# Optimization experiments

Hardware: AMD Instinct MI355X
Metric: run time of the kernel (lower is better)

The kernel has to match this reference:

```python
import jax, jax.numpy as jnp
import numpy as np

N_NODES = 50000
N_EDGES = 600000
DIM = 128
BN_EPS = 1e-5


def _gine_conv(x, src, dst, edge_attr, W, b):
    # message: relu(x_j + e_ij), gathered from source nodes
    m = jax.nn.relu(x[src] + edge_attr)              # [E, D]
    aggr = jax.ops.segment_sum(m, dst, num_segments=x.shape[0])  # [N, D]
    # eps = 0 (PyG default, train_eps=False): (1+eps)*x + aggr
    return (x + aggr) @ W.T + b


def _batchnorm(x, gamma, beta):
    mean = jnp.mean(x, axis=0)
    var = jnp.var(x, axis=0)
    return (x - mean) * jax.lax.rsqrt(var + BN_EPS) * gamma + beta


def setup_inputs() -> dict:
    key = jax.random.key(0)
    ks = jax.random.split(key, 16)
    scale = 1.0 / np.sqrt(DIM)
    inp = {
        "edge_index": jax.random.randint(ks[0], (2, N_EDGES), 0, N_NODES, dtype=jnp.int64 if jax.config.jax_enable_x64 else jnp.int32),
        "node_attr": jax.random.normal(ks[1], (N_NODES, DIM), dtype=jnp.float32),
        "edge_attr": jax.random.normal(ks[2], (N_EDGES, DIM), dtype=jnp.float32),
    }
    for i in range(3):
        inp[f"W{i+1}"] = jax.random.uniform(ks[3 + i], (DIM, DIM), jnp.float32, -scale, scale)
        inp[f"b{i+1}"] = jax.random.uniform(ks[6 + i], (DIM,), jnp.float32, -scale, scale)
        inp[f"gamma{i+1}"] = jnp.ones((DIM,), jnp.float32)
        inp[f"beta{i+1}"] = jnp.zeros((DIM,), jnp.float32)
    return inp


def reference(edge_index, node_attr, edge_attr,
              W1, b1, gamma1, beta1,
              W2, b2, gamma2, beta2,
              W3, b3, gamma3, beta3):
    src, dst = edge_index[0], edge_index[1]
    x = jax.nn.relu(_gine_conv(node_attr, src, dst, edge_attr, W1, b1))
    x = _batchnorm(x, gamma1, beta1)
    x = jax.nn.relu(_gine_conv(x, src, dst, edge_attr, W2, b2))
    x = _batchnorm(x, gamma2, beta2)
    x = jax.nn.relu(_gine_conv(x, src, dst, edge_attr, W3, b3))
    x = _batchnorm(x, gamma3, beta3)
    return x
```

## Files before the change

### kernel.cpp

```cpp
#include <hip/hip_runtime.h>
#include <stdint.h>

#define NN 50000
#define NE 600000
#define DIM 128
#define BN_EPS 1e-5f
#define NCHUNK ((NN + 255) / 256)

typedef __attribute__((ext_vector_type(8))) short bf16x8;
typedef __attribute__((ext_vector_type(4))) float f32x4;

__device__ __forceinline__ unsigned short f2b(float f) {
    unsigned u = __float_as_uint(f);
    u += 0x7FFF + ((u >> 16) & 1);
    return (unsigned short)(u >> 16);
}
__device__ __forceinline__ float b2f(unsigned short h) {
    return __uint_as_float((unsigned)h << 16);
}


__global__ __launch_bounds__(256) void zero_k(int* __restrict__ counts,
                                              double* __restrict__ gsum,
                                              double* __restrict__ gsumsq) {
    int i = blockIdx.x * 256 + threadIdx.x;
    if (i < NN) counts[i] = 0;
    if (i < DIM) { gsum[i] = 0.0; gsumsq[i] = 0.0; }
}

__global__ void count_k(const int* __restrict__ dst, int* __restrict__ counts, int E) {
    int i = blockIdx.x * 256 + threadIdx.x;
    if (i < E) atomicAdd(&counts[dst[i]], 1);
}

__global__ __launch_bounds__(256) void chunksum_k(const int* __restrict__ counts,
                                                  int* __restrict__ bsum) {
    __shared__ int lds[256];
    int i = blockIdx.x * 256 + threadIdx.x;
    lds[threadIdx.x] = (i < NN) ? counts[i] : 0;
    __syncthreads();
    for (int off = 128; off > 0; off >>= 1) {
        if (threadIdx.x < (unsigned)off) lds[threadIdx.x] += lds[threadIdx.x + off];
        __syncthreads();
    }
    if (threadIdx.x == 0) bsum[blockIdx.x] = lds[0];
}

__global__ __launch_bounds__(256) void chunkscan_k(const int* __restrict__ bsum,
                                                   int* __restrict__ bbase,
                                                   int* __restrict__ offsets) {
    __shared__ int lds[256];
    int t = threadIdx.x;
    int v = (t < NCHUNK) ? bsum[t] : 0;
    lds[t] = v;
    __syncthreads();
    for (int off = 1; off < 256; off <<= 1) {
        int a = (t >= (unsigned)off) ? lds[t - off] : 0;
        __syncthreads();
        lds[t] += a;
        __syncthreads();
    }
    if (t < NCHUNK) bbase[t] = lds[t] - v;
    if (t == 0) offsets[NN] = NE;
}

__global__ __launch_bounds__(256) void scatteroff_k(const int* __restrict__ counts,
                                                    const int* __restrict__ bbase,
                                                    int* __restrict__ offsets,
                                                    int* __restrict__ cursor) {
    __shared__ int lds[256];
    int t = threadIdx.x;
    int i = blockIdx.x * 256 + t;
    int v = (i < NN) ? counts[i] : 0;
    lds[t] = v;
    __syncthreads();
    for (int off = 1; off < 256; off <<= 1) {
        int a = (t >= (unsigned)off) ? lds[t - off] : 0;
        __syncthreads();
        lds[t] += a;
        __syncthreads();
    }
    if (i < NN) {
        int excl = bbase[blockIdx.x] + lds[t] - v;
        offsets[i] = excl;
        cursor[i] = excl;
    }
}

template <bool WEBF>
__global__ __launch_bounds__(256) void fillcvt_k(
        const int* __restrict__ dst, const int* __restrict__ src,
        const float* __restrict__ eattr, int* __restrict__ cursor,
        int* __restrict__ csrc, int* __restrict__ eidx,
        unsigned short* __restrict__ ebf) {
    int lane = threadIdx.x & 31;
    int g = blockIdx.x * 8 + (threadIdx.x >> 5);
    int base = g * 32;
    if (base >= NE) return;
    int i = base + lane;
    int d = dst[i];
    int p = atomicAdd(&cursor[d], 1);
    csrc[p] = src[i];
    if (!WEBF) { eidx[p] = i; return; }
    int f = lane * 4;
    for (int t = 0; t < 32; ++t) {
        int pt = __shfl(p, t, 32);
        float4 v = *(const float4*)(eattr + (size_t)(base + t) * DIM + f);
        ushort4 o = {f2b(v.x), f2b(v.y), f2b(v.z), f2b(v.w)};
        *(ushort4*)(ebf + (size_t)pt * DIM + f) = o;
    }
}

__global__ __launch_bounds__(256) void wcvt_k(const float* __restrict__ w0,
                                              const float* __restrict__ w1,
                                              const float* __restrict__ w2,
                                              unsigned short* __restrict__ whi,
                                              unsigned short* __restrict__ wlo) {
    int i = blockIdx.x * 256 + threadIdx.x;
    int which = i >> 12;
    int off = (i & 4095) * 4;
    const float* w = (which == 0) ? w0 : ((which == 1) ? w1 : w2);
    float4 v = *(const float4*)(w + off);
    ushort4 h = {f2b(v.x), f2b(v.y), f2b(v.z), f2b(v.w)};
    ushort4 l = {f2b(v.x - b2f(h.x)), f2b(v.y - b2f(h.y)),
                 f2b(v.z - b2f(h.z)), f2b(v.w - b2f(h.w))};
    *(ushort4*)(whi + (size_t)which * 16384 + off) = h;
    *(ushort4*)(wlo + (size_t)which * 16384 + off) = l;
}

template <int XMODE, int EMODE>
__global__ __launch_bounds__(256) void layer_k(
        const float* __restrict__ xf, const unsigned short* __restrict__ xb,
        const float* __restrict__ scale, const float* __restrict__ shift,
        const unsigned short* __restrict__ ebf, const float* __restrict__ eattr,
        const int* __restrict__ eidx, const int* __restrict__ offsets,
        const int* __restrict__ csrc,
        const unsigned short* __restrict__ whi, const unsigned short* __restrict__ wlo,
        const float* __restrict__ bias, unsigned short* __restrict__ yb,
        double* __restrict__ gsum, double* __restrict__ gsumsq) {
    __shared__ float sS[16][DIM + 4];
    __shared__ unsigned short ylds[16][136];

    int tid = threadIdx.x;
    int lane31 = tid & 31;
    int grp = tid >> 5;
    int n0 = blockIdx.x * 16;
    int f = lane31 * 4;

    float4 sc, sh;
    if (XMODE) {
        sc = *(const float4*)(scale + f);
        sh = *(const float4*)(shift + f);
    }

#pragma unroll
    for (int sub = 0; sub < 2; ++sub) {
        int n = n0 + grp * 2 + sub;
        float4 acc = make_float4(0.f, 0.f, 0.f, 0.f);
        int beg = offsets[n], end = offsets[n + 1];
        for (int b = beg; b < end; b += 32) {
            int kk = b + lane31;
            int s_l = (kk < end) ? csrc[kk] : 0;
            int e_l = 0;
            if (EMODE == 1) e_l = (kk < end) ? eidx[kk] : 0;
            int cnt = end - b;
            if (cnt > 32) cnt = 32;
#pragma unroll 4
            for (int t = 0; t < cnt; ++t) {
                int s = __shfl(s_l, t, 32);
                float4 ev;
                if (EMODE == 0) {
                    ushort4 eb = *(const ushort4*)(ebf + (size_t)(b + t) * DIM + f);
                    ev = make_float4(b2f(eb.x), b2f(eb.y), b2f(eb.z), b2f(eb.w));
                } else {
                    int e = __shfl(e_l, t, 32);
                    ev = *(const float4*)(eattr + (size_t)e * DIM + f);
                }
                float4 xv;
                if (XMODE == 0) {
                    xv = *(const float4*)(xf + (size_t)s * DIM + f);
                } else {
                    ushort4 u = *(const ushort4*)(xb + (size_t)s * DIM + f);
                    xv = make_float4(fmaf(b2f(u.x), sc.x, sh.x),
                                     fmaf(b2f(u.y), sc.y, sh.y),
                                     fmaf(b2f(u.z), sc.z, sh.z),
                                     fmaf(b2f(u.w), sc.w, sh.w));
                }
                acc.x += fmaxf(xv.x + ev.x, 0.f);
                acc.y += fmaxf(xv.y + ev.y, 0.f);
                acc.z += fmaxf(xv.z + ev.z, 0.f);
                acc.w += fmaxf(xv.w + ev.w, 0.f);
            }
        }
        float4 xn;
        if (XMODE == 0) {
            xn = *(const float4*)(xf + (size_t)n * DIM + f);
        } else {
            ushort4 u = *(const ushort4*)(xb + (size_t)n * DIM + f);
            xn = make_float4(fmaf(b2f(u.x), sc.x, sh.x), fmaf(b2f(u.y), sc.y, sh.y),
                             fmaf(b2f(u.z), sc.z, sh.z), fmaf(b2f(u.w), sc.w, sh.w));
        }
        float4 o = make_float4(xn.x + acc.x, xn.y + acc.y, xn.z + acc.z, xn.w + acc.w);
        *(float4*)(&sS[grp * 2 + sub][f]) = o;
    }
    __syncthreads();

    int wv = tid >> 6;
    int lane = tid & 63;
    int row = lane & 15;
    int kg = lane >> 4;
    int d0 = wv * 32;
    const unsigned short* bh = whi + (size_t)(d0 + row) * DIM + kg * 8;
    const unsigned short* bl = wlo + (size_t)(d0 + row) * DIM + kg * 8;

    f32x4 acc0 = {0.f, 0.f, 0.f, 0.f};
    f32x4 acc1 = {0.f, 0.f, 0.f, 0.f};
#pragma unroll
    for (int ks = 0; ks < 4; ++ks) {
        const float* ap = &sS[row][kg * 8 + ks * 32];
        bf16x8 a;
#pragma unroll
        for (int j = 0; j < 8; ++j) a[j] = (short)f2b(ap[j]);
        bf16x8 b0h = *(const bf16x8*)(bh + ks * 32);
        bf16x8 b0l = *(const bf16x8*)(bl + ks * 32);
        bf16x8 b1h = *(const bf16x8*)(bh + 16 * DIM + ks * 32);
        bf16x8 b1l = *(const bf16x8*)(bl + 16 * DIM + ks * 32);
        acc0 = __builtin_amdgcn_mfma_f32_16x16x32_bf16(a, b0h, acc0, 0, 0, 0);
        acc0 = __builtin_amdgcn_mfma_f32_16x16x32_bf16(a, b0l, acc0, 0, 0, 0);
        acc1 = __builtin_amdgcn_mfma_f32_16x16x32_bf16(a, b1h, acc1, 0, 0, 0);
        acc1 = __builtin_amdgcn_mfma_f32_16x16x32_bf16(a, b1l, acc1, 0, 0, 0);
    }

    float bias0 = bias[d0 + row];
    float bias1 = bias[d0 + 16 + row];
    float s0 = 0.f, q0 = 0.f, s1 = 0.f, q1 = 0.f;
#pragma unroll
    for (int r = 0; r < 4; ++r) {
        int m = kg * 4 + r;
        float y0 = fmaxf(acc0[r] + bias0, 0.f);
        float y1 = fmaxf(acc1[r] + bias1, 0.f);
        ylds[m][d0 + row] = f2b(y0);
        ylds[m][d0 + 16 + row] = f2b(y1);
        s0 += y0; q0 += y0 * y0;
        s1 += y1; q1 += y1 * y1;
    }
    s0 += __shfl_xor(s0, 16); s0 += __shfl_xor(s0, 32);
    q0 += __shfl_xor(q0, 16); q0 += __shfl_xor(q0, 32);
    s1 += __shfl_xor(s1, 16); s1 += __shfl_xor(s1, 32);
    q1 += __shfl_xor(q1, 16); q1 += __shfl_xor(q1, 32);
    if (kg == 0) {
        atomicAdd(&gsum[d0 + row], (double)s0);
        atomicAdd(&gsumsq[d0 + row], (double)q0);
        atomicAdd(&gsum[d0 + 16 + row], (double)s1);
        atomicAdd(&gsumsq[d0 + 16 + row], (double)q1);
    }
    __syncthreads();
    int nrow = tid >> 4, seg = tid & 15;
    *(float4*)(yb + (size_t)(n0 + nrow) * DIM + seg * 8) =
        *(const float4*)(&ylds[nrow][seg * 8]);
}

__global__ void finalize_k(double* __restrict__ gsum, double* __restrict__ gsumsq,
                           const float* __restrict__ gamma, const float* __restrict__ beta,
                           float* __restrict__ scale, float* __restrict__ shift) {
    int d = threadIdx.x;
    if (d < DIM) {
        double mean = gsum[d] * (1.0 / NN);
        double var = gsumsq[d] * (1.0 / NN) - mean * mean;
        float sc = gamma[d] * rsqrtf((float)var + BN_EPS);
        scale[d] = sc;
        shift[d] = beta[d] - (float)mean * sc;
        gsum[d] = 0.0;
        gsumsq[d] = 0.0;
    }
}

__global__ __launch_bounds__(256) void norm_out_k(
        const unsigned short* __restrict__ yb, const float* __restrict__ scale,
        const float* __restrict__ shift, float* __restrict__ out) {
    int i = blockIdx.x * 256 + threadIdx.x;
    int f = (i & 31) * 4;
    ushort4 y = *(const ushort4*)(yb + (size_t)i * 4);
    float4 sc = *(const float4*)(scale + f);
    float4 sh = *(const float4*)(shift + f);
    float4 o;
    o.x = fmaf(b2f(y.x), sc.x, sh.x);
    o.y = fmaf(b2f(y.y), sc.y, sh.y);
    o.z = fmaf(b2f(y.z), sc.z, sh.z);
    o.w = fmaf(b2f(y.w), sc.w, sh.w);
    ((float4*)out)[i] = o;
}


extern "C" void kernel_launch(void* const* d_in, const int* in_sizes, int n_in,
                              void* d_out, int out_size, void* d_ws, size_t ws_size,
                              hipStream_t stream) {
    const int* edge_index = (const int*)d_in[0];
    const int* srcs = edge_index;
    const int* dsts = edge_index + NE;
    const float* node_attr = (const float*)d_in[1];
    const float* eattr = (const float*)d_in[2];
    const float* Wp[3]    = {(const float*)d_in[3],  (const float*)d_in[7],  (const float*)d_in[11]};
    const float* bp[3]    = {(const float*)d_in[4],  (const float*)d_in[8],  (const float*)d_in[12]};
    const float* gammap[3]= {(const float*)d_in[5],  (const float*)d_in[9],  (const float*)d_in[13]};
    const float* betap[3] = {(const float*)d_in[6],  (const float*)d_in[10], (const float*)d_in[14]};

    size_t off = 0;
    char* base = (char*)d_ws;
    auto carve = [&](size_t bytes) -> void* {
        void* p = base + off;
        off += (bytes + 255) & ~(size_t)255;
        return p;
    };
    unsigned short* ybufA = (unsigned short*)carve((size_t)NN * DIM * 2);
    unsigned short* ybufB = (unsigned short*)carve((size_t)NN * DIM * 2);
    int* csrc    = (int*)carve((size_t)NE * 4);
    int* eidx    = (int*)carve((size_t)NE * 4);
    int* offsets = (int*)carve((size_t)(NN + 1) * 4);
    int* cursor  = (int*)carve((size_t)NN * 4);
    int* bsum    = (int*)carve((size_t)NCHUNK * 4);
    int* bbase   = (int*)carve((size_t)NCHUNK * 4);
    int* counts  = (int*)carve((size_t)NN * 4);
    double* gsum = (double*)carve(DIM * 8);
    double* gsumsq = (double*)carve(DIM * 8);
    float* scb   = (float*)carve(3 * DIM * 4);
    float* shb   = (float*)carve(3 * DIM * 4);
    unsigned short* whi = (unsigned short*)carve(3 * DIM * DIM * 2);
    unsigned short* wlo = (unsigned short*)carve(3 * DIM * DIM * 2);
    int use_ebf = (off + (size_t)NE * DIM * 2 <= ws_size);
    unsigned short* ebf = use_ebf ? (unsigned short*)carve((size_t)NE * DIM * 2) : nullptr;

    zero_k<<<NCHUNK, 256, 0, stream>>>(counts, gsum, gsumsq);
    count_k<<<(NE + 255) / 256, 256, 0, stream>>>(dsts, counts, NE);
    chunksum_k<<<NCHUNK, 256, 0, stream>>>(counts, bsum);
    chunkscan_k<<<1, 256, 0, stream>>>(bsum, bbase, offsets);
    scatteroff_k<<<NCHUNK, 256, 0, stream>>>(counts, bbase, offsets, cursor);
    if (use_ebf)
        fillcvt_k<true><<<(NE / 32 + 7) / 8, 256, 0, stream>>>(dsts, srcs, eattr, cursor,
                                                               csrc, eidx, ebf);
    else
        fillcvt_k<false><<<(NE / 32 + 7) / 8, 256, 0, stream>>>(dsts, srcs, eattr, cursor,
                                                                csrc, eidx, nullptr);
    wcvt_k<<<48, 256, 0, stream>>>(Wp[0], Wp[1], Wp[2], whi, wlo);

    if (use_ebf)
        layer_k<0, 0><<<NN / 16, 256, 0, stream>>>(node_attr, nullptr, nullptr, nullptr,
                                                   ebf, eattr, eidx, offsets, csrc,
                                                   whi, wlo, bp[0], ybufA, gsum, gsumsq);
    else
        layer_k<0, 1><<<NN / 16, 256, 0, stream>>>(node_attr, nullptr, nullptr, nullptr,
                                                   nullptr, eattr, eidx, offsets, csrc,
                                                   whi, wlo, bp[0], ybufA, gsum, gsumsq);
    finalize_k<<<1, DIM, 0, stream>>>(gsum, gsumsq, gammap[0], betap[0], scb, shb);

    unsigned short* xin = ybufA;
    unsigned short* yout = ybufB;
    for (int l = 1; l < 3; ++l) {
        const float* sc = scb + (l - 1) * DIM;
        const float* sh = shb + (l - 1) * DIM;
        if (use_ebf)
            layer_k<1, 0><<<NN / 16, 256, 0, stream>>>(nullptr, xin, sc, sh,
                                                       ebf, eattr, eidx, offsets, csrc,
                                                       whi + l * DIM * DIM, wlo + l * DIM * DIM,
                                                       bp[l], yout, gsum, gsumsq);
        else
            layer_k<1, 1><<<NN / 16, 256, 0, stream>>>(nullptr, xin, sc, sh,
                                                       nullptr, eattr, eidx, offsets, csrc,
                                                       whi + l * DIM * DIM, wlo + l * DIM * DIM,
                                                       bp[l], yout, gsum, gsumsq);
        finalize_k<<<1, DIM, 0, stream>>>(gsum, gsumsq, gammap[l], betap[l],
                                          scb + l * DIM, shb + l * DIM);
        unsigned short* t = xin; xin = yout; yout = t;
    }
    norm_out_k<<<NN * DIM / 4 / 256, 256, 0, stream>>>(xin, scb + 2 * DIM, shb + 2 * DIM,
                                                       (float*)d_out);
}
```

Measured before the change: 491.8 us.

## Fuse BN finalize into layer kernels, merge init kernels, prequantize node features

Drops the per-layer finalize kernels. Each layer kernel, and the output kernel, now recompute the batch-norm scale and shift from per-layer double sums, which are kept in separate buffers so nothing has to be zeroed again. The zero and weight-convert kernels merge into one init kernel, which also converts node_attr to bf16 so the first layer gathers half the bytes. Edge loads and stores use nontemporal hints. The cost is redundant stats computation in every thread, and bf16 rounding of the first layer's input, which changes precision.

```diff
diff --git a/kernel.cpp b/kernel.cpp
--- a/kernel.cpp
+++ b/kernel.cpp
@@ -6,9 +6,11 @@
 #define DIM 128
 #define BN_EPS 1e-5f
 #define NCHUNK ((NN + 255) / 256)
+#define NABBLK (NN * DIM / 4 / 256)
 
 typedef __attribute__((ext_vector_type(8))) short bf16x8;
 typedef __attribute__((ext_vector_type(4))) float f32x4;
+typedef __attribute__((ext_vector_type(2))) unsigned int u32x2;
 
 __device__ __forceinline__ unsigned short f2b(float f) {
     unsigned u = __float_as_uint(f);
@@ -20,13 +22,42 @@
 }
 
 
-__global__ __launch_bounds__(256) void zero_k(int* __restrict__ counts,
+__global__ __launch_bounds__(256) void init_k(int* __restrict__ counts,
                                               double* __restrict__ gsum,
-                                              double* __restrict__ gsumsq) {
-    int i = blockIdx.x * 256 + threadIdx.x;
-    if (i < NN) counts[i] = 0;
-    if (i < DIM) { gsum[i] = 0.0; gsumsq[i] = 0.0; }
-}
+                                              double* __restrict__ gsumsq,
+                                              const float* __restrict__ w0,
+                                              const float* __restrict__ w1,
+                                              const float* __restrict__ w2,
+                                              unsigned short* __restrict__ whi,
+                                              unsigned short* __restrict__ wlo,
+                                              const float* __restrict__ xf,
+                                              unsigned short* __restrict__ nabf) {
+    int bid = blockIdx.x;
+    if (bid < NCHUNK) {
+        int i = bid * 256 + threadIdx.x;
+        if (i < NN) counts[i] = 0;
+        if (i < 3 * DIM) { gsum[i] = 0.0; gsumsq[i] = 0.0; }
+    } else if (bid < NCHUNK + 48) {
+        int i = (bid - NCHUNK) * 256 + threadIdx.x;
+        int which = i >> 12;
+        int off = (i & 4095) * 4;
+        const float* w = (which == 0) ? w0 : ((which == 1) ? w1 : w2);
+        float4 v = *(const float4*)(w + off);
+        ushort4 h = {f2b(v.x), f2b(v.y), f2b(v.z), f2b(v.w)};
+        ushort4 l = {f2b(v.x - b2f(h.x)), f2b(v.y - b2f(h.y)),
+                     f2b(v.z - b2f(h.z)), f2b(v.w - b2f(h.w))};
+        *(ushort4*)(whi + (size_t)which * 16384 + off) = h;
+        *(ushort4*)(wlo + (size_t)which * 16384 + off) = l;
+    } else {
+        int idx = (bid - NCHUNK - 48) * 256 + threadIdx.x;
+        f32x4 v = __builtin_nontemporal_load((const f32x4*)(xf + (size_t)idx * 4));
+        u32x2 o;
+        o[0] = (unsigned)f2b(v[0]) | ((unsigned)f2b(v[1]) << 16);
+        o[1] = (unsigned)f2b(v[2]) | ((unsigned)f2b(v[3]) << 16);
+        __builtin_nontemporal_store(o, (u32x2*)(nabf + (size_t)idx * 4));
+    }
+}
+
 
 __global__ void count_k(const int* __restrict__ dst, int* __restrict__ counts, int E) {
     int i = blockIdx.x * 256 + threadIdx.x;
@@ -103,41 +134,29 @@
     csrc[p] = src[i];
     if (!WEBF) { eidx[p] = i; return; }
     int f = lane * 4;
+#pragma unroll 4
     for (int t = 0; t < 32; ++t) {
         int pt = __shfl(p, t, 32);
-        float4 v = *(const float4*)(eattr + (size_t)(base + t) * DIM + f);
-        ushort4 o = {f2b(v.x), f2b(v.y), f2b(v.z), f2b(v.w)};
-        *(ushort4*)(ebf + (size_t)pt * DIM + f) = o;
-    }
-}
-
-__global__ __launch_bounds__(256) void wcvt_k(const float* __restrict__ w0,
-                                              const float* __restrict__ w1,
-                                              const float* __restrict__ w2,
-                                              unsigned short* __restrict__ whi,
-                                              unsigned short* __restrict__ wlo) {
-    int i = blockIdx.x * 256 + threadIdx.x;
-    int which = i >> 12;
-    int off = (i & 4095) * 4;
-    const float* w = (which == 0) ? w0 : ((which == 1) ? w1 : w2);
-    float4 v = *(const float4*)(w + off);
-    ushort4 h = {f2b(v.x), f2b(v.y), f2b(v.z), f2b(v.w)};
-    ushort4 l = {f2b(v.x - b2f(h.x)), f2b(v.y - b2f(h.y)),
-                 f2b(v.z - b2f(h.z)), f2b(v.w - b2f(h.w))};
-    *(ushort4*)(whi + (size_t)which * 16384 + off) = h;
-    *(ushort4*)(wlo + (size_t)which * 16384 + off) = l;
+        f32x4 v = __builtin_nontemporal_load(
+            (const f32x4*)(eattr + (size_t)(base + t) * DIM + f));
+        u32x2 o;
+        o[0] = (unsigned)f2b(v[0]) | ((unsigned)f2b(v[1]) << 16);
+        o[1] = (unsigned)f2b(v[2]) | ((unsigned)f2b(v[3]) << 16);
+        __builtin_nontemporal_store(o, (u32x2*)(ebf + (size_t)pt * DIM + f));
+    }
 }
 
 template <int XMODE, int EMODE>
 __global__ __launch_bounds__(256) void layer_k(
-        const float* __restrict__ xf, const unsigned short* __restrict__ xb,
-        const float* __restrict__ scale, const float* __restrict__ shift,
+        const unsigned short* __restrict__ xb,
+        const double* __restrict__ gs_prev, const double* __restrict__ gq_prev,
+        const float* __restrict__ gamma_prev, const float* __restrict__ beta_prev,
         const unsigned short* __restrict__ ebf, const float* __restrict__ eattr,
         const int* __restrict__ eidx, const int* __restrict__ offsets,
         const int* __restrict__ csrc,
         const unsigned short* __restrict__ whi, const unsigned short* __restrict__ wlo,
         const float* __restrict__ bias, unsigned short* __restrict__ yb,
-        double* __restrict__ gsum, double* __restrict__ gsumsq) {
+        double* __restrict__ gs_cur, double* __restrict__ gq_cur) {
     __shared__ float sS[16][DIM + 4];
     __shared__ unsigned short ylds[16][136];
 
@@ -147,10 +166,17 @@
     int n0 = blockIdx.x * 16;
     int f = lane31 * 4;
 
-    float4 sc, sh;
-    if (XMODE) {
-        sc = *(const float4*)(scale + f);
-        sh = *(const float4*)(shift + f);
+    f32x4 sc, sh;
+    if (XMODE == 1) {
+#pragma unroll
+        for (int j = 0; j < 4; ++j) {
+            int d = f + j;
+            double mean = gs_prev[d] * (1.0 / NN);
+            double var = gq_prev[d] * (1.0 / NN) - mean * mean;
+            float s = gamma_prev[d] * rsqrtf((float)var + BN_EPS);
+            sc[j] = s;
+            sh[j] = beta_prev[d] - (float)mean * s;
+        }
     }
 
 #pragma unroll
@@ -170,21 +196,25 @@
                 int s = __shfl(s_l, t, 32);
                 float4 ev;
                 if (EMODE == 0) {
-                    ushort4 eb = *(const ushort4*)(ebf + (size_t)(b + t) * DIM + f);
-                    ev = make_float4(b2f(eb.x), b2f(eb.y), b2f(eb.z), b2f(eb.w));
+                    u32x2 ew = __builtin_nontemporal_load(
+                        (const u32x2*)(ebf + (size_t)(b + t) * DIM + f));
+                    ev = make_float4(b2f((unsigned short)(ew[0] & 0xFFFFu)),
+                                     b2f((unsigned short)(ew[0] >> 16)),
+                                     b2f((unsigned short)(ew[1] & 0xFFFFu)),
+                                     b2f((unsigned short)(ew[1] >> 16)));
                 } else {
                     int e = __shfl(e_l, t, 32);
                     ev = *(const float4*)(eattr + (size_t)e * DIM + f);
                 }
+                ushort4 u = *(const ushort4*)(xb + (size_t)s * DIM + f);
                 float4 xv;
-                if (XMODE == 0) {
-                    xv = *(const float4*)(xf + (size_t)s * DIM + f);
+                if (XMODE == 1) {
+                    xv = make_float4(fmaf(b2f(u.x), sc[0], sh[0]),
+                                     fmaf(b2f(u.y), sc[1], sh[1]),
+                                     fmaf(b2f(u.z), sc[2], sh[2]),
+                                     fmaf(b2f(u.w), sc[3], sh[3]));
                 } else {
-                    ushort4 u = *(const ushort4*)(xb + (size_t)s * DIM + f);
-                    xv = make_float4(fmaf(b2f(u.x), sc.x, sh.x),
-                                     fmaf(b2f(u.y), sc.y, sh.y),
-                                     fmaf(b2f(u.z), sc.z, sh.z),
-                                     fmaf(b2f(u.w), sc.w, sh.w));
+                    xv = make_float4(b2f(u.x), b2f(u.y), b2f(u.z), b2f(u.w));
                 }
                 acc.x += fmaxf(xv.x + ev.x, 0.f);
                 acc.y += fmaxf(xv.y + ev.y, 0.f);
@@ -192,13 +222,13 @@
                 acc.w += fmaxf(xv.w + ev.w, 0.f);
             }
         }
+        ushort4 u = *(const ushort4*)(xb + (size_t)n * DIM + f);
         float4 xn;
-        if (XMODE == 0) {
-            xn = *(const float4*)(xf + (size_t)n * DIM + f);
+        if (XMODE == 1) {
+            xn = make_float4(fmaf(b2f(u.x), sc[0], sh[0]), fmaf(b2f(u.y), sc[1], sh[1]),
+                             fmaf(b2f(u.z), sc[2], sh[2]), fmaf(b2f(u.w), sc[3], sh[3]));
         } else {
-            ushort4 u = *(const ushort4*)(xb + (size_t)n * DIM + f);
-            xn = make_float4(fmaf(b2f(u.x), sc.x, sh.x), fmaf(b2f(u.y), sc.y, sh.y),
-                             fmaf(b2f(u.z), sc.z, sh.z), fmaf(b2f(u.w), sc.w, sh.w));
+            xn = make_float4(b2f(u.x), b2f(u.y), b2f(u.z), b2f(u.w));
         }
         float4 o = make_float4(xn.x + acc.x, xn.y + acc.y, xn.z + acc.z, xn.w + acc.w);
         *(float4*)(&sS[grp * 2 + sub][f]) = o;
@@ -249,10 +279,10 @@
     s1 += __shfl_xor(s1, 16); s1 += __shfl_xor(s1, 32);
     q1 += __shfl_xor(q1, 16); q1 += __shfl_xor(q1, 32);
     if (kg == 0) {
-        atomicAdd(&gsum[d0 + row], (double)s0);
-        atomicAdd(&gsumsq[d0 + row], (double)q0);
-        atomicAdd(&gsum[d0 + 16 + row], (double)s1);
-        atomicAdd(&gsumsq[d0 + 16 + row], (double)q1);
+        atomicAdd(&gs_cur[d0 + row], (double)s0);
+        atomicAdd(&gq_cur[d0 + row], (double)q0);
+        atomicAdd(&gs_cur[d0 + 16 + row], (double)s1);
+        atomicAdd(&gq_cur[d0 + 16 + row], (double)q1);
     }
     __syncthreads();
     int nrow = tid >> 4, seg = tid & 15;
@@ -260,34 +290,29 @@
         *(const float4*)(&ylds[nrow][seg * 8]);
 }
 
-__global__ void finalize_k(double* __restrict__ gsum, double* __restrict__ gsumsq,
-                           const float* __restrict__ gamma, const float* __restrict__ beta,
-                           float* __restrict__ scale, float* __restrict__ shift) {
-    int d = threadIdx.x;
-    if (d < DIM) {
-        double mean = gsum[d] * (1.0 / NN);
-        double var = gsumsq[d] * (1.0 / NN) - mean * mean;
-        float sc = gamma[d] * rsqrtf((float)var + BN_EPS);
-        scale[d] = sc;
-        shift[d] = beta[d] - (float)mean * sc;
-        gsum[d] = 0.0;
-        gsumsq[d] = 0.0;
-    }
-}
-
 __global__ __launch_bounds__(256) void norm_out_k(
-        const unsigned short* __restrict__ yb, const float* __restrict__ scale,
-        const float* __restrict__ shift, float* __restrict__ out) {
+        const unsigned short* __restrict__ yb,
+        const double* __restrict__ gs, const double* __restrict__ gq,
+        const float* __restrict__ gamma, const float* __restrict__ beta,
+        float* __restrict__ out) {
     int i = blockIdx.x * 256 + threadIdx.x;
     int f = (i & 31) * 4;
+    float sc[4], sh[4];
+#pragma unroll
+    for (int j = 0; j < 4; ++j) {
+        int d = f + j;
+        double mean = gs[d] * (1.0 / NN);
+        double var = gq[d] * (1.0 / NN) - mean * mean;
+        float s = gamma[d] * rsqrtf((float)var + BN_EPS);
+        sc[j] = s;
+        sh[j] = beta[d] - (float)mean * s;
+    }
     ushort4 y = *(const ushort4*)(yb + (size_t)i * 4);
-    float4 sc = *(const float4*)(scale + f);
-    float4 sh = *(const float4*)(shift + f);
     float4 o;
-    o.x = fmaf(b2f(y.x), sc.x, sh.x);
-    o.y = fmaf(b2f(y.y), sc.y, sh.y);
-    o.z = fmaf(b2f(y.z), sc.z, sh.z);
-    o.w = fmaf(b2f(y.w), sc.w, sh.w);
+    o.x = fmaf(b2f(y.x), sc[0], sh[0]);
+    o.y = fmaf(b2f(y.y), sc[1], sh[1]);
+    o.z = fmaf(b2f(y.z), sc[2], sh[2]);
+    o.w = fmaf(b2f(y.w), sc[3], sh[3]);
     ((float4*)out)[i] = o;
 }
 
@@ -314,6 +339,7 @@
     };
     unsigned short* ybufA = (unsigned short*)carve((size_t)NN * DIM * 2);
     unsigned short* ybufB = (unsigned short*)carve((size_t)NN * DIM * 2);
+    unsigned short* nabf = (unsigned short*)carve((size_t)NN * DIM * 2);
     int* csrc    = (int*)carve((size_t)NE * 4);
     int* eidx    = (int*)carve((size_t)NE * 4);
     int* offsets = (int*)carve((size_t)(NN + 1) * 4);
@@ -321,16 +347,16 @@
     int* bsum    = (int*)carve((size_t)NCHUNK * 4);
     int* bbase   = (int*)carve((size_t)NCHUNK * 4);
     int* counts  = (int*)carve((size_t)NN * 4);
-    double* gsum = (double*)carve(DIM * 8);
-    double* gsumsq = (double*)carve(DIM * 8);
-    float* scb   = (float*)carve(3 * DIM * 4);
-    float* shb   = (float*)carve(3 * DIM * 4);
+    double* gsum = (double*)carve(3 * DIM * 8);
+    double* gsumsq = (double*)carve(3 * DIM * 8);
     unsigned short* whi = (unsigned short*)carve(3 * DIM * DIM * 2);
     unsigned short* wlo = (unsigned short*)carve(3 * DIM * DIM * 2);
     int use_ebf = (off + (size_t)NE * DIM * 2 <= ws_size);
     unsigned short* ebf = use_ebf ? (unsigned short*)carve((size_t)NE * DIM * 2) : nullptr;
 
-    zero_k<<<NCHUNK, 256, 0, stream>>>(counts, gsum, gsumsq);
+    init_k<<<NCHUNK + 48 + NABBLK, 256, 0, stream>>>(counts, gsum, gsumsq,
+                                                     Wp[0], Wp[1], Wp[2], whi, wlo,
+                                                     node_attr, nabf);
     count_k<<<(NE + 255) / 256, 256, 0, stream>>>(dsts, counts, NE);
     chunksum_k<<<NCHUNK, 256, 0, stream>>>(counts, bsum);
     chunkscan_k<<<1, 256, 0, stream>>>(bsum, bbase, offsets);
@@ -341,37 +367,37 @@
     else
         fillcvt_k<false><<<(NE / 32 + 7) / 8, 256, 0, stream>>>(dsts, srcs, eattr, cursor,
                                                                 csrc, eidx, nullptr);
-    wcvt_k<<<48, 256, 0, stream>>>(Wp[0], Wp[1], Wp[2], whi, wlo);
 
     if (use_ebf)
-        layer_k<0, 0><<<NN / 16, 256, 0, stream>>>(node_attr, nullptr, nullptr, nullptr,
+        layer_k<2, 0><<<NN / 16, 256, 0, stream>>>(nabf, nullptr, nullptr, nullptr, nullptr,
                                                    ebf, eattr, eidx, offsets, csrc,
                                                    whi, wlo, bp[0], ybufA, gsum, gsumsq);
     else
-        layer_k<0, 1><<<NN / 16, 256, 0, stream>>>(node_attr, nullptr, nullptr, nullptr,
+        layer_k<2, 1><<<NN / 16, 256, 0, stream>>>(nabf, nullptr, nullptr, nullptr, nullptr,
                                                    nullptr, eattr, eidx, offsets, csrc,
                                                    whi, wlo, bp[0], ybufA, gsum, gsumsq);
-    finalize_k<<<1, DIM, 0, stream>>>(gsum, gsumsq, gammap[0], betap[0], scb, shb);
 
     unsigned short* xin = ybufA;
     unsigned short* yout = ybufB;
     for (int l = 1; l < 3; ++l) {
-        const float* sc = scb + (l - 1) * DIM;
-        const float* sh = shb + (l - 1) * DIM;
+        const double* gsp = gsum + (l - 1) * DIM;
+        const double* gqp = gsumsq + (l - 1) * DIM;
         if (use_ebf)
-            layer_k<1, 0><<<NN / 16, 256, 0, stream>>>(nullptr, xin, sc, sh,
+            layer_k<1, 0><<<NN / 16, 256, 0, stream>>>(xin, gsp, gqp,
+                                                       gammap[l - 1], betap[l - 1],
                                                        ebf, eattr, eidx, offsets, csrc,
                                                        whi + l * DIM * DIM, wlo + l * DIM * DIM,
-                                                       bp[l], yout, gsum, gsumsq);
+                                                       bp[l], yout,
+                                                       gsum + l * DIM, gsumsq + l * DIM);
         else
-            layer_k<1, 1><<<NN / 16, 256, 0, stream>>>(nullptr, xin, sc, sh,
+            layer_k<1, 1><<<NN / 16, 256, 0, stream>>>(xin, gsp, gqp,
+                                                       gammap[l - 1], betap[l - 1],
                                                        nullptr, eattr, eidx, offsets, csrc,
                                                        whi + l * DIM * DIM, wlo + l * DIM * DIM,
-                                                       bp[l], yout, gsum, gsumsq);
-        finalize_k<<<1, DIM, 0, stream>>>(gsum, gsumsq, gammap[l], betap[l],
-                                          scb + l * DIM, shb + l * DIM);
+                                                       bp[l], yout,
+                                                       gsum + l * DIM, gsumsq + l * DIM);
         unsigned short* t = xin; xin = yout; yout = t;
     }
-    norm_out_k<<<NN * DIM / 4 / 256, 256, 0, stream>>>(xin, scb + 2 * DIM, shb + 2 * DIM,
-                                                       (float*)d_out);
-}
+    norm_out_k<<<NN * DIM / 4 / 256, 256, 0, stream>>>(xin, gsum + 2 * DIM, gsumsq + 2 * DIM,
+                                                       gammap[2], betap[2], (float*)d_out);
+}
```

After: 491.9 us. No clear change (+0.0%).
